# Performance work log

Hardware: AMD Instinct MI355X
Metric: run time of the kernel (lower is better)

## Reference

```python
import jax, jax.numpy as jnp
import numpy as np

N, E, H, C, IN = 50000, 500000, 4, 64, 256


def setup_inputs() -> dict:
    key = jax.random.key(0)
    ks = jax.random.split(key, 16)
    sW = 1.0 / np.sqrt(IN)
    sA = 1.0 / np.sqrt(C)
    inp = {
        "x": jax.random.normal(ks[0], (N, IN), jnp.float32),
        "edge_index": jax.random.randint(ks[1], (2, E), 0, N, jnp.int64 if jax.config.jax_enable_x64 else jnp.int32),
        "W1": jax.random.normal(ks[2], (IN, H * C), jnp.float32) * sW,
        "as1": jax.random.normal(ks[3], (H, C), jnp.float32) * sA,
        "ad1": jax.random.normal(ks[4], (H, C), jnp.float32) * sA,
        "b1": jnp.zeros((H * C,), jnp.float32),
        "W2": jax.random.normal(ks[5], (H * C, H * C), jnp.float32) * sW,
        "as2": jax.random.normal(ks[6], (H, C), jnp.float32) * sA,
        "ad2": jax.random.normal(ks[7], (H, C), jnp.float32) * sA,
        "b2": jnp.zeros((H * C,), jnp.float32),
        "WN": jax.random.normal(ks[8], (H * C, H * C), jnp.float32) * sW,
        "asN": jax.random.normal(ks[9], (H, C), jnp.float32) * sA,
        "adN": jax.random.normal(ks[10], (H, C), jnp.float32) * sA,
        "bN": jnp.zeros((H * C,), jnp.float32),
    }
    return inp


def _gat_conv(x, src, dst, W, a_src, a_dst, b, n_nodes):
    # x: [N, F_in]; src/dst: [E'] (self-loops included); W: [F_in, H*C]
    Hh, Cc = a_src.shape
    h = (x @ W).reshape(n_nodes, Hh, Cc)                      # [N,H,C]
    e_src = jnp.einsum("nhc,hc->nh", h, a_src)                # [N,H]
    e_dst = jnp.einsum("nhc,hc->nh", h, a_dst)
    e = jax.nn.leaky_relu(e_src[src] + e_dst[dst], 0.2)       # [E',H]
    m = jax.lax.stop_gradient(jax.ops.segment_max(e, dst, num_segments=n_nodes))
    ex = jnp.exp(e - m[dst])
    denom = jax.ops.segment_sum(ex, dst, num_segments=n_nodes)
    alpha = ex / (denom[dst] + 1e-16)                         # [E',H]
    out = jax.ops.segment_sum(h[src] * alpha[:, :, None], dst, num_segments=n_nodes)
    return out.reshape(n_nodes, Hh * Cc) + b


def reference(x, edge_index, W1, as1, ad1, b1, W2, as2, ad2, b2, WN, asN, adN, bN):
    n = x.shape[0]
    loops = jnp.arange(n, dtype=edge_index.dtype)
    src = jnp.concatenate([edge_index[0], loops])  # PyG GATConv add_self_loops=True
    dst = jnp.concatenate([edge_index[1], loops])
    inp = x
    h = jax.nn.relu(_gat_conv(x, src, dst, W1, as1, ad1, b1, n)) + inp
    h = jax.nn.relu(_gat_conv(h, src, dst, W2, as2, ad2, b2, n))
    h = _gat_conv(h, src, dst, WN, asN, adN, bN, n)
    # eval mode: F.dropout is identity
    return jax.nn.relu(h + inp)
```

## Files before the change

kernel.cpp:

```cpp
#include <hip/hip_runtime.h>
#include <hip/hip_bf16.h>
#include <math.h>

typedef short short8 __attribute__((ext_vector_type(8)));
typedef float f32x4 __attribute__((ext_vector_type(4)));

static __device__ __forceinline__ float bf2f(__hip_bfloat16 h) { return __bfloat162float(h); }
static __device__ __forceinline__ float bfu(unsigned short u) {
    union { unsigned int i; float f; } c; c.i = ((unsigned int)u) << 16; return c.f;
}


__global__ void k_cast_bf16(const float* __restrict__ in, __hip_bfloat16* __restrict__ out, int n) {
    int i4 = (blockIdx.x * blockDim.x + threadIdx.x) * 4;
    if (i4 >= n) return;
    float4 f = *(const float4*)(in + i4);
    union { ushort u[4]; uint2 v; } o;
    __hip_bfloat16 h0 = __float2bfloat16(f.x); o.u[0] = *(ushort*)&h0;
    __hip_bfloat16 h1 = __float2bfloat16(f.y); o.u[1] = *(ushort*)&h1;
    __hip_bfloat16 h2 = __float2bfloat16(f.z); o.u[2] = *(ushort*)&h2;
    __hip_bfloat16 h3 = __float2bfloat16(f.w); o.u[3] = *(ushort*)&h3;
    *(uint2*)(out + i4) = o.v;
}

__global__ void k_wt_cast(const float* __restrict__ W, __hip_bfloat16* __restrict__ Wt) {
    int n = blockIdx.x, k = threadIdx.x;
    Wt[n * 256 + k] = __float2bfloat16(W[k * 256 + n]);
}


__global__ void k_set1(int* a, int n) {
    int i = blockIdx.x * blockDim.x + threadIdx.x;
    if (i < n) a[i] = 1;
}

__global__ void k_hist(const int* __restrict__ dstv, int* __restrict__ cnt, int E) {
    int i = blockIdx.x * blockDim.x + threadIdx.x;
    if (i < E) atomicAdd(&cnt[dstv[i]], 1);
}

__global__ void k_scan1(const int* __restrict__ cnt, int* __restrict__ excl, int* __restrict__ bsum, int n) {
    __shared__ int s[256];
    int i = blockIdx.x * 256 + threadIdx.x;
    int v = (i < n) ? cnt[i] : 0;
    s[threadIdx.x] = v;
    __syncthreads();
    for (int off = 1; off < 256; off <<= 1) {
        int t = (threadIdx.x >= off) ? s[threadIdx.x - off] : 0;
        __syncthreads();
        s[threadIdx.x] += t;
        __syncthreads();
    }
    if (i < n) excl[i] = s[threadIdx.x] - v;
    if (threadIdx.x == 255) bsum[blockIdx.x] = s[255];
}

__global__ void k_scan2(const int* __restrict__ bsum, int* __restrict__ boff, int nb) {
    __shared__ int s[256];
    int carry = 0;
    for (int base = 0; base < nb; base += 256) {
        int i = base + threadIdx.x;
        int v = (i < nb) ? bsum[i] : 0;
        s[threadIdx.x] = v;
        __syncthreads();
        for (int off = 1; off < 256; off <<= 1) {
            int t = (threadIdx.x >= off) ? s[threadIdx.x - off] : 0;
            __syncthreads();
            s[threadIdx.x] += t;
            __syncthreads();
        }
        if (i < nb) boff[i] = carry + s[threadIdx.x] - v;
        carry += s[255];
        __syncthreads();
    }
}

__global__ void k_scan3(const int* __restrict__ excl, const int* __restrict__ boff,
                        int* __restrict__ rowptr, int* __restrict__ cursor, int n, int Etot) {
    int i = blockIdx.x * blockDim.x + threadIdx.x;
    if (i < n) {
        int v = excl[i] + boff[i >> 8];
        rowptr[i] = v;
        cursor[i] = v;
    }
    if (i == 0) rowptr[n] = Etot;
}

__global__ void k_scatter(const int* __restrict__ srcv, const int* __restrict__ dstv,
                          int* __restrict__ cursor, int* __restrict__ colsrc, int E, int Nn) {
    int i = blockIdx.x * blockDim.x + threadIdx.x;
    if (i < E) {
        int pos = atomicAdd(&cursor[dstv[i]], 1);
        colsrc[pos] = srcv[i];
    } else if (i < E + Nn) {
        int nn = i - E;
        int pos = atomicAdd(&cursor[nn], 1);
        colsrc[pos] = nn;
    }
}


__global__ __launch_bounds__(256) void k_gemm(const __hip_bfloat16* __restrict__ A,
                                              const __hip_bfloat16* __restrict__ Wt,
                                              __hip_bfloat16* __restrict__ C,
                                              const float* __restrict__ a_src,
                                              const float* __restrict__ a_dst,
                                              float* __restrict__ es,
                                              float* __restrict__ ed, int M) {
    __shared__ __align__(16) char As[64 * 128];
    __shared__ __align__(16) char Bs[256 * 128];
    int tid = threadIdx.x;
    int w = tid >> 6, l = tid & 63;
    int m0 = blockIdx.x * 64;
    f32x4 acc[4][4];
#pragma unroll
    for (int a = 0; a < 4; ++a)
#pragma unroll
        for (int b = 0; b < 4; ++b) acc[a][b] = (f32x4){0.f, 0.f, 0.f, 0.f};

    for (int bk = 0; bk < 256; bk += 64) {
        __syncthreads();
#pragma unroll
        for (int i = 0; i < 2; ++i) {
            int c = tid + 256 * i;
            int row = c >> 3, ko = c & 7;
            int rg = m0 + row;
            uint4 v = {0u, 0u, 0u, 0u};
            if (rg < M) v = *(const uint4*)((const char*)A + (size_t)rg * 512 + bk * 2 + ko * 16);
            int off = (ko * 16) ^ ((row & 7) << 4);
            *(uint4*)(As + row * 128 + off) = v;
        }
#pragma unroll
        for (int i = 0; i < 8; ++i) {
            int c = tid + 256 * i;
            int row = c >> 3, ko = c & 7;
            uint4 v = *(const uint4*)((const char*)Wt + (size_t)row * 512 + bk * 2 + ko * 16);
            int off = (ko * 16) ^ ((row & 7) << 4);
            *(uint4*)(Bs + row * 128 + off) = v;
        }
        __syncthreads();
        int lo = l & 15, hi = l >> 4;
#pragma unroll
        for (int kk = 0; kk < 2; ++kk) {
            int koff = kk * 64 + hi * 16;
            short8 af[4], bfr[4];
#pragma unroll
            for (int mi = 0; mi < 4; ++mi) {
                int row = mi * 16 + lo;
                af[mi] = *(const short8*)(As + row * 128 + (koff ^ ((row & 7) << 4)));
            }
#pragma unroll
            for (int ni = 0; ni < 4; ++ni) {
                int row = w * 64 + ni * 16 + lo;
                bfr[ni] = *(const short8*)(Bs + row * 128 + (koff ^ ((row & 7) << 4)));
            }
#pragma unroll
            for (int mi = 0; mi < 4; ++mi)
#pragma unroll
                for (int ni = 0; ni < 4; ++ni)
                    acc[mi][ni] = __builtin_amdgcn_mfma_f32_16x16x32_bf16(af[mi], bfr[ni], acc[mi][ni], 0, 0, 0);
        }
    }
    int lo = l & 15, hi = l >> 4;
#pragma unroll
    for (int mi = 0; mi < 4; ++mi) {
#pragma unroll
        for (int r = 0; r < 4; ++r) {
            int rg = m0 + mi * 16 + hi * 4 + r;
            if (rg < M) {
#pragma unroll
                for (int ni = 0; ni < 4; ++ni) {
                    int col = w * 64 + ni * 16 + lo;
                    C[(size_t)rg * 256 + col] = __float2bfloat16(acc[mi][ni][r]);
                }
            }
        }
    }
    float avv[4], adv[4];
#pragma unroll
    for (int ni = 0; ni < 4; ++ni) {
        avv[ni] = a_src[w * 64 + ni * 16 + lo];
        adv[ni] = a_dst[w * 64 + ni * 16 + lo];
    }
#pragma unroll
    for (int mi = 0; mi < 4; ++mi) {
#pragma unroll
        for (int r = 0; r < 4; ++r) {
            int rg = m0 + mi * 16 + hi * 4 + r;
            float s1 = 0.f, s2 = 0.f;
#pragma unroll
            for (int ni = 0; ni < 4; ++ni) {
                s1 += acc[mi][ni][r] * avv[ni];
                s2 += acc[mi][ni][r] * adv[ni];
            }
#pragma unroll
            for (int mk = 1; mk < 16; mk <<= 1) {
                s1 += __shfl_xor(s1, mk, 64);
                s2 += __shfl_xor(s2, mk, 64);
            }
            if (lo == 0 && rg < M) {
                es[rg * 4 + w] = s1;
                ed[rg * 4 + w] = s2;
            }
        }
    }
}


__global__ __launch_bounds__(256) void k_aggregate(const __hip_bfloat16* __restrict__ hW,
                            const int* __restrict__ rowptr,
                            const int* __restrict__ colsrc, const float* __restrict__ es,
                            const float* __restrict__ edv_, const float* __restrict__ bias,
                            const float* __restrict__ xres, __hip_bfloat16* __restrict__ outbf,
                            float* __restrict__ outf, int mode, int Nn) {
    __shared__ int s_lds[4][64];
    __shared__ float p_lds[4][64][4];
    int wid = threadIdx.x >> 6;
    int n = blockIdx.x * 4 + wid;
    if (n >= Nn) return;
    int l = threadIdx.x & 63;
    int h = l >> 4;
    int r0 = rowptr[n];
    int deg = rowptr[n + 1] - r0;
    float4 ed4 = *(const float4*)(edv_ + n * 4);

    float denom = 0.f;
    float a0 = 0.f, a1 = 0.f, a2 = 0.f, a3 = 0.f;
    const ushort* hw = (const ushort*)hW;

    for (int base = 0; base < deg; base += 64) {
        int cn = min(64, deg - base);
        asm volatile("s_waitcnt lgkmcnt(0)" ::: "memory");
        if (l < cn) {
            int s = colsrc[r0 + base + l];
            float4 e4 = *(const float4*)(es + (size_t)s * 4);
            s_lds[wid][l] = s;
            float t0 = e4.x + ed4.x; t0 = fmaxf(t0, 0.2f * t0);
            float t1 = e4.y + ed4.y; t1 = fmaxf(t1, 0.2f * t1);
            float t2 = e4.z + ed4.z; t2 = fmaxf(t2, 0.2f * t2);
            float t3 = e4.w + ed4.w; t3 = fmaxf(t3, 0.2f * t3);
            float4 p4;
            p4.x = __expf(t0); p4.y = __expf(t1);
            p4.z = __expf(t2); p4.w = __expf(t3);
            *(float4*)&p_lds[wid][l][0] = p4;
        }
        asm volatile("s_waitcnt lgkmcnt(0)" ::: "memory");

        int jj = 0;
        for (; jj + 8 <= cn; jj += 8) {
            int sv[8]; float pv[8];
#pragma unroll
            for (int u = 0; u < 8; ++u) {
                sv[u] = s_lds[wid][jj + u];
                pv[u] = p_lds[wid][jj + u][h];
            }
            uint2 hv[8];
#pragma unroll
            for (int u = 0; u < 8; ++u)
                hv[u] = *(const uint2*)(hw + (size_t)sv[u] * 256 + l * 4);
#pragma unroll
            for (int u = 0; u < 8; ++u) {
                float p = pv[u];
                denom += p;
                a0 += p * bfu((ushort)(hv[u].x & 0xffff));
                a1 += p * bfu((ushort)(hv[u].x >> 16));
                a2 += p * bfu((ushort)(hv[u].y & 0xffff));
                a3 += p * bfu((ushort)(hv[u].y >> 16));
            }
        }
        for (; jj < cn; ++jj) {
            int s = s_lds[wid][jj];
            float p = p_lds[wid][jj][h];
            uint2 hv = *(const uint2*)(hw + (size_t)s * 256 + l * 4);
            denom += p;
            a0 += p * bfu((ushort)(hv.x & 0xffff));
            a1 += p * bfu((ushort)(hv.x >> 16));
            a2 += p * bfu((ushort)(hv.y & 0xffff));
            a3 += p * bfu((ushort)(hv.y >> 16));
        }
    }

    float inv = 1.f / (denom + 1e-16f);
    int idx = n * 256 + l * 4;
    float4 b4 = *(const float4*)(bias + l * 4);
    float v0 = a0 * inv + b4.x;
    float v1 = a1 * inv + b4.y;
    float v2 = a2 * inv + b4.z;
    float v3 = a3 * inv + b4.w;

    if (mode == 2) {
        float4 x4 = *(const float4*)(xres + idx);
        float4 o;
        o.x = fmaxf(v0 + x4.x, 0.f);
        o.y = fmaxf(v1 + x4.y, 0.f);
        o.z = fmaxf(v2 + x4.z, 0.f);
        o.w = fmaxf(v3 + x4.w, 0.f);
        *(float4*)(outf + idx) = o;
    } else {
        v0 = fmaxf(v0, 0.f); v1 = fmaxf(v1, 0.f);
        v2 = fmaxf(v2, 0.f); v3 = fmaxf(v3, 0.f);
        if (mode == 0) {
            float4 x4 = *(const float4*)(xres + idx);
            v0 += x4.x; v1 += x4.y; v2 += x4.z; v3 += x4.w;
        }
        union { ushort u[4]; uint2 v; } o;
        __hip_bfloat16 h0 = __float2bfloat16(v0); o.u[0] = *(ushort*)&h0;
        __hip_bfloat16 h1 = __float2bfloat16(v1); o.u[1] = *(ushort*)&h1;
        __hip_bfloat16 h2 = __float2bfloat16(v2); o.u[2] = *(ushort*)&h2;
        __hip_bfloat16 h3 = __float2bfloat16(v3); o.u[3] = *(ushort*)&h3;
        *(uint2*)((ushort*)outbf + idx) = o.v;
    }
}


extern "C" void kernel_launch(void* const* d_in, const int* in_sizes, int n_in,
                              void* d_out, int out_size, void* d_ws, size_t ws_size,
                              hipStream_t stream) {
    const float* x  = (const float*)d_in[0];
    const int* ei   = (const int*)d_in[1];
    const float* W1 = (const float*)d_in[2];
    const float* as1 = (const float*)d_in[3];
    const float* ad1 = (const float*)d_in[4];
    const float* b1  = (const float*)d_in[5];
    const float* W2  = (const float*)d_in[6];
    const float* as2 = (const float*)d_in[7];
    const float* ad2 = (const float*)d_in[8];
    const float* b2  = (const float*)d_in[9];
    const float* WN  = (const float*)d_in[10];
    const float* asN = (const float*)d_in[11];
    const float* adN = (const float*)d_in[12];
    const float* bN  = (const float*)d_in[13];

    int Nn = in_sizes[0] / 256;
    int E = in_sizes[1] / 2;
    const int* srcv = ei;
    const int* dstv = ei + E;
    int Etot = E + Nn;

    char* p = (char*)d_ws;
    auto alloc = [&](size_t bytes) {
        char* r = p;
        p += (bytes + 255) & ~(size_t)255;
        return r;
    };
    __hip_bfloat16* xbf  = (__hip_bfloat16*)alloc((size_t)Nn * 256 * 2);
    __hip_bfloat16* Pbf  = (__hip_bfloat16*)alloc((size_t)Nn * 256 * 2);
    __hip_bfloat16* Qbf  = (__hip_bfloat16*)alloc((size_t)Nn * 256 * 2);
    __hip_bfloat16* hWbf = (__hip_bfloat16*)alloc((size_t)Nn * 256 * 2);
    __hip_bfloat16* Wt1  = (__hip_bfloat16*)alloc(256 * 256 * 2);
    __hip_bfloat16* Wt2  = (__hip_bfloat16*)alloc(256 * 256 * 2);
    __hip_bfloat16* Wt3  = (__hip_bfloat16*)alloc(256 * 256 * 2);
    float* esrc = (float*)alloc((size_t)Nn * 4 * 4);
    float* edst = (float*)alloc((size_t)Nn * 4 * 4);
    int* cnt    = (int*)alloc((size_t)Nn * 4);
    int* excl   = (int*)alloc((size_t)Nn * 4);
    int* rowptr = (int*)alloc((size_t)(Nn + 1) * 4);
    int* cursor = (int*)alloc((size_t)Nn * 4);
    int* bsum   = (int*)alloc(4096);
    int* boff   = (int*)alloc(4096);
    int* colsrc = (int*)alloc((size_t)Etot * 4);

    int nb = (Nn + 255) / 256;

    k_cast_bf16<<<(Nn * 256 / 4 + 255) / 256, 256, 0, stream>>>(x, xbf, Nn * 256);
    k_wt_cast<<<256, 256, 0, stream>>>(W1, Wt1);
    k_wt_cast<<<256, 256, 0, stream>>>(W2, Wt2);
    k_wt_cast<<<256, 256, 0, stream>>>(WN, Wt3);

    k_set1<<<nb, 256, 0, stream>>>(cnt, Nn);
    k_hist<<<(E + 255) / 256, 256, 0, stream>>>(dstv, cnt, E);
    k_scan1<<<nb, 256, 0, stream>>>(cnt, excl, bsum, Nn);
    k_scan2<<<1, 256, 0, stream>>>(bsum, boff, nb);
    k_scan3<<<nb, 256, 0, stream>>>(excl, boff, rowptr, cursor, Nn, Etot);
    k_scatter<<<(Etot + 255) / 256, 256, 0, stream>>>(srcv, dstv, cursor, colsrc, E, Nn);

    int gg = (Nn + 63) / 64;
    int ga = (Nn + 3) / 4;

    k_gemm<<<gg, 256, 0, stream>>>(xbf, Wt1, hWbf, as1, ad1, esrc, edst, Nn);
    k_aggregate<<<ga, 256, 0, stream>>>(hWbf, rowptr, colsrc, esrc, edst, b1, x, Pbf, nullptr, 0, Nn);
    k_gemm<<<gg, 256, 0, stream>>>(Pbf, Wt2, hWbf, as2, ad2, esrc, edst, Nn);
    k_aggregate<<<ga, 256, 0, stream>>>(hWbf, rowptr, colsrc, esrc, edst, b2, x, Qbf, nullptr, 1, Nn);
    k_gemm<<<gg, 256, 0, stream>>>(Qbf, Wt3, hWbf, asN, adN, esrc, edst, Nn);
    k_aggregate<<<ga, 256, 0, stream>>>(hWbf, rowptr, colsrc, esrc, edst, bN, x, nullptr, (float*)d_out, 2, Nn);
}
```

Baseline: 318.6 us.

## Enlarge GEMM M-tile to 128 rows and simplify aggregation to direct per-lane loads

The GEMM block now covers 128 rows instead of 64, so each loaded weight tile is reused across twice as many A rows, at the cost of more accumulator registers and LDS. The aggregation kernel drops its LDS staging of neighbor indices and precomputed exponentials. Each lane now loads colsrc and its own head's es value directly in groups of 8, padding the tail with a dummy neighbor that gets zero weight. This removes LDS traffic and waitcnt barriers but recomputes the exp per lane and issues redundant scalar loads across lanes.

New measurement: 348.2 us. +9.3%, slower.

```diff
diff --git a/kernel.cpp b/kernel.cpp
--- a/kernel.cpp
+++ b/kernel.cpp
@@ -5,7 +5,6 @@
 typedef short short8 __attribute__((ext_vector_type(8)));
 typedef float f32x4 __attribute__((ext_vector_type(4)));
 
-static __device__ __forceinline__ float bf2f(__hip_bfloat16 h) { return __bfloat162float(h); }
 static __device__ __forceinline__ float bfu(unsigned short u) {
     union { unsigned int i; float f; } c; c.i = ((unsigned int)u) << 16; return c.f;
 }
@@ -107,21 +106,21 @@
                                               const float* __restrict__ a_dst,
                                               float* __restrict__ es,
                                               float* __restrict__ ed, int M) {
-    __shared__ __align__(16) char As[64 * 128];
+    __shared__ __align__(16) char As[128 * 128];
     __shared__ __align__(16) char Bs[256 * 128];
     int tid = threadIdx.x;
     int w = tid >> 6, l = tid & 63;
-    int m0 = blockIdx.x * 64;
-    f32x4 acc[4][4];
-#pragma unroll
-    for (int a = 0; a < 4; ++a)
+    int m0 = blockIdx.x * 128;
+    f32x4 acc[8][4];
+#pragma unroll
+    for (int a = 0; a < 8; ++a)
 #pragma unroll
         for (int b = 0; b < 4; ++b) acc[a][b] = (f32x4){0.f, 0.f, 0.f, 0.f};
 
     for (int bk = 0; bk < 256; bk += 64) {
         __syncthreads();
 #pragma unroll
-        for (int i = 0; i < 2; ++i) {
+        for (int i = 0; i < 4; ++i) {
             int c = tid + 256 * i;
             int row = c >> 3, ko = c & 7;
             int rg = m0 + row;
@@ -143,27 +142,25 @@
 #pragma unroll
         for (int kk = 0; kk < 2; ++kk) {
             int koff = kk * 64 + hi * 16;
-            short8 af[4], bfr[4];
-#pragma unroll
-            for (int mi = 0; mi < 4; ++mi) {
-                int row = mi * 16 + lo;
-                af[mi] = *(const short8*)(As + row * 128 + (koff ^ ((row & 7) << 4)));
-            }
+            short8 bfr[4];
 #pragma unroll
             for (int ni = 0; ni < 4; ++ni) {
                 int row = w * 64 + ni * 16 + lo;
                 bfr[ni] = *(const short8*)(Bs + row * 128 + (koff ^ ((row & 7) << 4)));
             }
 #pragma unroll
-            for (int mi = 0; mi < 4; ++mi)
+            for (int mi = 0; mi < 8; ++mi) {
+                int row = mi * 16 + lo;
+                short8 af = *(const short8*)(As + row * 128 + (koff ^ ((row & 7) << 4)));
 #pragma unroll
                 for (int ni = 0; ni < 4; ++ni)
-                    acc[mi][ni] = __builtin_amdgcn_mfma_f32_16x16x32_bf16(af[mi], bfr[ni], acc[mi][ni], 0, 0, 0);
+                    acc[mi][ni] = __builtin_amdgcn_mfma_f32_16x16x32_bf16(af, bfr[ni], acc[mi][ni], 0, 0, 0);
+            }
         }
     }
     int lo = l & 15, hi = l >> 4;
 #pragma unroll
-    for (int mi = 0; mi < 4; ++mi) {
+    for (int mi = 0; mi < 8; ++mi) {
 #pragma unroll
         for (int r = 0; r < 4; ++r) {
             int rg = m0 + mi * 16 + hi * 4 + r;
@@ -183,7 +180,7 @@
         adv[ni] = a_dst[w * 64 + ni * 16 + lo];
     }
 #pragma unroll
-    for (int mi = 0; mi < 4; ++mi) {
+    for (int mi = 0; mi < 8; ++mi) {
 #pragma unroll
         for (int r = 0; r < 4; ++r) {
             int rg = m0 + mi * 16 + hi * 4 + r;
@@ -213,70 +210,42 @@
                             const float* __restrict__ edv_, const float* __restrict__ bias,
                             const float* __restrict__ xres, __hip_bfloat16* __restrict__ outbf,
                             float* __restrict__ outf, int mode, int Nn) {
-    __shared__ int s_lds[4][64];
-    __shared__ float p_lds[4][64][4];
-    int wid = threadIdx.x >> 6;
-    int n = blockIdx.x * 4 + wid;
+    int n = blockIdx.x * 4 + (threadIdx.x >> 6);
     if (n >= Nn) return;
     int l = threadIdx.x & 63;
     int h = l >> 4;
     int r0 = rowptr[n];
     int deg = rowptr[n + 1] - r0;
-    float4 ed4 = *(const float4*)(edv_ + n * 4);
+    float edv = edv_[n * 4 + h];
 
     float denom = 0.f;
     float a0 = 0.f, a1 = 0.f, a2 = 0.f, a3 = 0.f;
     const ushort* hw = (const ushort*)hW;
-
-    for (int base = 0; base < deg; base += 64) {
-        int cn = min(64, deg - base);
-        asm volatile("s_waitcnt lgkmcnt(0)" ::: "memory");
-        if (l < cn) {
-            int s = colsrc[r0 + base + l];
-            float4 e4 = *(const float4*)(es + (size_t)s * 4);
-            s_lds[wid][l] = s;
-            float t0 = e4.x + ed4.x; t0 = fmaxf(t0, 0.2f * t0);
-            float t1 = e4.y + ed4.y; t1 = fmaxf(t1, 0.2f * t1);
-            float t2 = e4.z + ed4.z; t2 = fmaxf(t2, 0.2f * t2);
-            float t3 = e4.w + ed4.w; t3 = fmaxf(t3, 0.2f * t3);
-            float4 p4;
-            p4.x = __expf(t0); p4.y = __expf(t1);
-            p4.z = __expf(t2); p4.w = __expf(t3);
-            *(float4*)&p_lds[wid][l][0] = p4;
-        }
-        asm volatile("s_waitcnt lgkmcnt(0)" ::: "memory");
-
-        int jj = 0;
-        for (; jj + 8 <= cn; jj += 8) {
-            int sv[8]; float pv[8];
-#pragma unroll
-            for (int u = 0; u < 8; ++u) {
-                sv[u] = s_lds[wid][jj + u];
-                pv[u] = p_lds[wid][jj + u][h];
-            }
-            uint2 hv[8];
-#pragma unroll
-            for (int u = 0; u < 8; ++u)
-                hv[u] = *(const uint2*)(hw + (size_t)sv[u] * 256 + l * 4);
-#pragma unroll
-            for (int u = 0; u < 8; ++u) {
-                float p = pv[u];
-                denom += p;
-                a0 += p * bfu((ushort)(hv[u].x & 0xffff));
-                a1 += p * bfu((ushort)(hv[u].x >> 16));
-                a2 += p * bfu((ushort)(hv[u].y & 0xffff));
-                a3 += p * bfu((ushort)(hv[u].y >> 16));
-            }
-        }
-        for (; jj < cn; ++jj) {
-            int s = s_lds[wid][jj];
-            float p = p_lds[wid][jj][h];
-            uint2 hv = *(const uint2*)(hw + (size_t)s * 256 + l * 4);
+    int sfb = colsrc[r0];
+
+    for (int base = 0; base < deg; base += 8) {
+        int sv[8];
+#pragma unroll
+        for (int u = 0; u < 8; ++u)
+            sv[u] = (base + u < deg) ? colsrc[r0 + base + u] : sfb;
+        float ev[8];
+#pragma unroll
+        for (int u = 0; u < 8; ++u)
+            ev[u] = es[(size_t)sv[u] * 4 + h];
+        uint2 hv[8];
+#pragma unroll
+        for (int u = 0; u < 8; ++u)
+            hv[u] = *(const uint2*)(hw + (size_t)sv[u] * 256 + l * 4);
+#pragma unroll
+        for (int u = 0; u < 8; ++u) {
+            float t = ev[u] + edv;
+            t = fmaxf(t, 0.2f * t);
+            float p = (base + u < deg) ? __expf(t) : 0.f;
             denom += p;
-            a0 += p * bfu((ushort)(hv.x & 0xffff));
-            a1 += p * bfu((ushort)(hv.x >> 16));
-            a2 += p * bfu((ushort)(hv.y & 0xffff));
-            a3 += p * bfu((ushort)(hv.y >> 16));
+            a0 += p * bfu((ushort)(hv[u].x & 0xffff));
+            a1 += p * bfu((ushort)(hv[u].x >> 16));
+            a2 += p * bfu((ushort)(hv[u].y & 0xffff));
+            a3 += p * bfu((ushort)(hv[u].y >> 16));
         }
     }
 
@@ -374,7 +343,7 @@
     k_scan3<<<nb, 256, 0, stream>>>(excl, boff, rowptr, cursor, Nn, Etot);
     k_scatter<<<(Etot + 255) / 256, 256, 0, stream>>>(srcv, dstv, cursor, colsrc, E, Nn);
 
-    int gg = (Nn + 63) / 64;
+    int gg = (Nn + 127) / 128;
     int ga = (Nn + 3) / 4;
 
     k_gemm<<<gg, 256, 0, stream>>>(xbf, Wt1, hWbf, as1, ad1, esrc, edst, Nn);
```
